# Optimization experiments

Hardware: AMD Instinct MI355X
Metric: run time of the kernel (lower is better)

## Reference

```python
import jax, jax.numpy as jnp
import numpy as np

EPS_LN = 1e-5
EPS_BN = 1e-5
NUM_HEADS = 8


def _gelu(x):
    return jax.nn.gelu(x, approximate=False)


def _ln(x, w, b):
    # LayerNorm over last (channel) dim, eps=1e-5 (torch default)
    mu = jnp.mean(x, axis=-1, keepdims=True)
    var = jnp.mean((x - mu) ** 2, axis=-1, keepdims=True)
    return (x - mu) / jnp.sqrt(var + EPS_LN) * w + b


def _bn(x, g, b):
    # eval-mode BatchNorm2d on NCHW with running_mean=0, running_var=1
    scale = g * (1.0 + EPS_BN) ** -0.5
    return x * scale[None, :, None, None] + b[None, :, None, None]


def _conv1x1(x, w):
    # x: [B,C,H,W], w: [O,C]
    return jnp.einsum('bchw,oc->bohw', x, w)


def _unfold3(x, r):
    # nn.Unfold(kernel=3, dilation=r, padding=r): gather 3x3 dilated neighborhoods
    B, C, H, W = x.shape
    xp = jnp.pad(x, ((0, 0), (0, 0), (r, r), (r, r)))
    pats = [xp[:, :, i * r:i * r + H, j * r:j * r + W] for i in range(3) for j in range(3)]
    return jnp.stack(pats, axis=2)  # [B,C,9,H,W]


def _atrous_attn(q, k, v, num_heads, r):
    # per-pixel local attention: q [B,C,H,W] attends to 9 dilated neighbors of k/v
    B, C, H, W = q.shape
    hd = C // num_heads
    scale = hd ** -0.5
    qh = q.reshape(B, num_heads, hd, H, W)
    kp = _unfold3(k, r).reshape(B, num_heads, hd, 9, H, W)
    attn = jax.nn.softmax(jnp.einsum('bnchw,bnckhw->bnkhw', qh, kp) * scale, axis=2)
    vp = _unfold3(v, r).reshape(B, num_heads, hd, 9, H, W)
    out = jnp.einsum('bnkhw,bnckhw->bnchw', attn, vp)
    return out.reshape(B, C, H, W).transpose(0, 2, 3, 1)  # [B,H,W,C]


def _window_attn(x_bhwc, qkv_w, proj_w, proj_b, num_heads, r):
    xc = x_bhwc.transpose(0, 3, 1, 2)
    C = xc.shape[1]
    qkv = _conv1x1(xc, qkv_w)  # [B,3C,H,W], order q|k|v
    out = _atrous_attn(qkv[:, :C], qkv[:, C:2 * C], qkv[:, 2 * C:], num_heads, r)
    return jnp.einsum('bhwc,oc->bhwo', out, proj_w) + proj_b


def _mlp(x_bhwc, c1_w, c1_b, bn1_g, bn1_b, dw_w, dw_b, bn2_g, bn2_b, c2_w, c2_b, bn3_g, bn3_b):
    xc = x_bhwc.transpose(0, 3, 1, 2)
    h = _bn(_gelu(_conv1x1(xc, c1_w) + c1_b[None, :, None, None]), bn1_g, bn1_b)
    dw = jax.lax.conv_general_dilated(h, dw_w, (1, 1), 'SAME',
                                      feature_group_count=h.shape[1],
                                      dimension_numbers=('NCHW', 'OIHW', 'NCHW'))
    dw = dw + dw_b[None, :, None, None]
    h = _bn(_gelu(dw + h), bn2_g, bn2_b)
    out = _bn(_conv1x1(h, c2_w) + c2_b[None, :, None, None], bn3_g, bn3_b)
    return out.transpose(0, 2, 3, 1)


def reference(x, ln1_w, ln1_b, ln2_w, ln2_b,
              qkv1_w, proj1_w, proj1_b, qkv2_w, proj2_w, proj2_b, qkv3_w, proj3_w, proj3_b,
              tc_conv_w, tc_conv_b, tc_bn1_g, tc_bn1_b, tc_pool_w, tc_bn2_g, tc_bn2_b,
              tc_trans_w, tc_trans_b, tc_bn3_g, tc_bn3_b,
              mlp_c1_w, mlp_c1_b, mlp_bn1_g, mlp_bn1_b, mlp_dw_w, mlp_dw_b,
              mlp_bn2_g, mlp_bn2_b, mlp_c2_w, mlp_c2_b, mlp_bn3_g, mlp_bn3_b):
    tx = x.transpose(0, 2, 3, 1)  # [B,H,W,C]
    n1 = _ln(tx, ln1_w, ln1_b)
    t1 = tx + _window_attn(n1, qkv1_w, proj1_w, proj1_b, NUM_HEADS, 1)
    t2 = tx + _window_attn(n1, qkv2_w, proj2_w, proj2_b, NUM_HEADS, 2)
    t3 = tx + _window_attn(n1, qkv3_w, proj3_w, proj3_b, NUM_HEADS, 3)
    # Trans_conv: ASPP-style fusion
    xc1 = jax.nn.relu(_bn(_conv1x1(x, tc_conv_w) + tc_conv_b[None, :, None, None], tc_bn1_g, tc_bn1_b))
    pool = jnp.mean(x, axis=(2, 3), keepdims=True)
    pool = jax.nn.relu(_bn(_conv1x1(pool, tc_pool_w), tc_bn2_g, tc_bn2_b))
    pool = jnp.broadcast_to(pool, x.shape)  # bilinear upsample of a 1x1 map == broadcast
    cat = jnp.concatenate([xc1, t1.transpose(0, 3, 1, 2), t2.transpose(0, 3, 1, 2),
                           t3.transpose(0, 3, 1, 2), pool], axis=1)  # [B,5C,H,W]
    tr = jax.nn.relu(_bn(_conv1x1(cat, tc_trans_w) + tc_trans_b[None, :, None, None],
                         tc_bn3_g, tc_bn3_b)).transpose(0, 2, 3, 1)  # [B,H,W,C]
    tr = tr + _mlp(_ln(tr, ln2_w, ln2_b), mlp_c1_w, mlp_c1_b, mlp_bn1_g, mlp_bn1_b,
                   mlp_dw_w, mlp_dw_b, mlp_bn2_g, mlp_bn2_b, mlp_c2_w, mlp_c2_b,
                   mlp_bn3_g, mlp_bn3_b)
    return tr.transpose(0, 3, 1, 2)  # [B,C,H,W]


def setup_inputs():
    key = jax.random.key(0)
    B, C, H, W = 4, 256, 64, 64
    HID = 4 * C
    ks = iter(jax.random.split(key, 64))

    def nrm(shape, scale=0.02):
        return jax.random.normal(next(ks), shape, dtype=jnp.float32) * scale

    inp = {
        'x': jax.random.normal(next(ks), (B, C, H, W), dtype=jnp.float32),
        'ln1_w': jnp.ones((C,), jnp.float32), 'ln1_b': jnp.zeros((C,), jnp.float32),
        'ln2_w': jnp.ones((C,), jnp.float32), 'ln2_b': jnp.zeros((C,), jnp.float32),
    }
    for i in (1, 2, 3):
        inp[f'qkv{i}_w'] = nrm((3 * C, C))
        inp[f'proj{i}_w'] = nrm((C, C))
        inp[f'proj{i}_b'] = jnp.zeros((C,), jnp.float32)
    inp.update(
        tc_conv_w=nrm((C, C)), tc_conv_b=jnp.zeros((C,), jnp.float32),
        tc_bn1_g=jnp.ones((C,), jnp.float32), tc_bn1_b=jnp.zeros((C,), jnp.float32),
        tc_pool_w=nrm((C, C)),
        tc_bn2_g=jnp.ones((C,), jnp.float32), tc_bn2_b=jnp.zeros((C,), jnp.float32),
        tc_trans_w=nrm((C, 5 * C)), tc_trans_b=jnp.zeros((C,), jnp.float32),
        tc_bn3_g=jnp.ones((C,), jnp.float32), tc_bn3_b=jnp.zeros((C,), jnp.float32),
        mlp_c1_w=nrm((HID, C)), mlp_c1_b=jnp.zeros((HID,), jnp.float32),
        mlp_bn1_g=jnp.ones((HID,), jnp.float32), mlp_bn1_b=jnp.zeros((HID,), jnp.float32),
        mlp_dw_w=nrm((HID, 1, 3, 3), 0.1), mlp_dw_b=jnp.zeros((HID,), jnp.float32),
        mlp_bn2_g=jnp.ones((HID,), jnp.float32), mlp_bn2_b=jnp.zeros((HID,), jnp.float32),
        mlp_c2_w=nrm((C, HID)), mlp_c2_b=jnp.zeros((C,), jnp.float32),
        mlp_bn3_g=jnp.ones((C,), jnp.float32), mlp_bn3_b=jnp.zeros((C,), jnp.float32),
    )
    return inp
```

## Files before the change

### kernel.cpp

```cpp
#include <hip/hip_runtime.h>

#define N_PIX 16384
#define CDIM  256
#define HIDD  1024
#define BNS   0.9999950000374997f

typedef __attribute__((ext_vector_type(8))) short  short8;
typedef __attribute__((ext_vector_type(4))) float  f32x4;
typedef __attribute__((ext_vector_type(4))) int    int4v;
typedef __attribute__((ext_vector_type(2))) int    int2v;

__device__ __forceinline__ float b2f(unsigned short u){
  unsigned int x = ((unsigned int)u) << 16; float f;
  __builtin_memcpy(&f, &x, 4); return f;
}
__device__ __forceinline__ unsigned short f2b(float f){
  unsigned int x; __builtin_memcpy(&x, &f, 4);
  unsigned int r = (x + 0x7fffu + ((x >> 16) & 1u)) >> 16;
  return (unsigned short)r;
}
__device__ __forceinline__ float geluf(float x){
  return 0.5f * x * (1.0f + erff(x * 0.70710678118654752f));
}

typedef const __attribute__((address_space(1))) unsigned int* gas_t;
typedef __attribute__((address_space(3))) unsigned int*       las_t;
__device__ __forceinline__ void gload16(const void* g, void* l){
  __builtin_amdgcn_global_load_lds((gas_t)g, (las_t)l, 16, 0, 0);
}

__global__ __launch_bounds__(256) void k_cvt_all(
    const float* __restrict__ s0, const float* __restrict__ s1, const float* __restrict__ s2,
    const float* __restrict__ s3, const float* __restrict__ s4, const float* __restrict__ s5,
    const float* __restrict__ s6, const float* __restrict__ s7, const float* __restrict__ s8,
    const float* __restrict__ s9, unsigned short* __restrict__ wb){
  const float* srcs[10] = {s0,s1,s2,s3,s4,s5,s6,s7,s8,s9};
  const int n[10]   = {196608,196608,196608,65536,65536,65536,65536,327680,262144,262144};
  const int off[10] = {0,196608,393216,589824,655360,720896,786432,851968,1179648,1441792};
  int seg = blockIdx.y;
  int i = (blockIdx.x * 256 + threadIdx.x) * 8;
  if (i >= n[seg]) return;
  const float* src = srcs[seg];
  unsigned short* dst = wb + off[seg];
  f32x4 a = *(const f32x4*)(src + i);
  f32x4 b = *(const f32x4*)(src + i + 4);
  unsigned short o[8];
  #pragma unroll
  for (int j = 0; j < 4; ++j){ o[j] = f2b(a[j]); o[4 + j] = f2b(b[j]); }
  *(int4v*)(dst + i) = *(int4v*)o;
}

__global__ __launch_bounds__(256) void k_dwwT(const float* __restrict__ dww,
                                              unsigned short* __restrict__ dwwT){
  int i = blockIdx.x * 256 + threadIdx.x;
  if (i >= 9216) return;
  int kk = i >> 10, c = i & 1023;
  dwwT[i] = f2b(dww[c * 9 + kk]);
}

__global__ __launch_bounds__(256) void k_transpose(const float* __restrict__ x,
                                                   unsigned short* __restrict__ xpm,
                                                   float* __restrict__ xpm32){
  __shared__ __align__(16) float tile[64][65];
  int b = blockIdx.z, c0 = blockIdx.y * 64, p0 = blockIdx.x * 64;
  int t = threadIdx.x;
  int r = t >> 3, k = t & 7;
  for (int s = 0; s < 2; ++s){
    int rr = r + s * 32;
    const float* src = x + (((size_t)(b * CDIM + c0 + rr)) << 12) + p0 + k * 8;
    f32x4 a = *(const f32x4*)src;
    f32x4 c = *(const f32x4*)(src + 4);
    #pragma unroll
    for (int j = 0; j < 4; ++j){ tile[rr][k * 8 + j] = a[j]; tile[rr][k * 8 + 4 + j] = c[j]; }
  }
  __syncthreads();
  for (int s = 0; s < 2; ++s){
    int pr = r + s * 32;
    float tf[8];
    unsigned short tb[8];
    #pragma unroll
    for (int j = 0; j < 8; ++j){ tf[j] = tile[k * 8 + j][pr]; tb[j] = f2b(tf[j]); }
    size_t rowoff = ((size_t)(b * 4096 + p0 + pr)) << 8;
    *(int4v*)(xpm + rowoff + c0 + k * 8) = *(int4v*)tb;
    *(f32x4*)(xpm32 + rowoff + c0 + k * 8)     = *(f32x4*)&tf[0];
    *(f32x4*)(xpm32 + rowoff + c0 + k * 8 + 4) = *(f32x4*)&tf[4];
  }
}

template<typename IT>
__global__ __launch_bounds__(256) void k_ln(const IT* __restrict__ in,
    const float* __restrict__ w, const float* __restrict__ bia,
    unsigned short* __restrict__ out){
  int row  = blockIdx.x * 4 + (threadIdx.x >> 6);
  int lane = threadIdx.x & 63;
  float v[4];
  const IT* p = in + (size_t)row * CDIM + lane * 4;
  if constexpr (sizeof(IT) == 2){
    int2v d = *(const int2v*)p;
    unsigned short tmp[4]; __builtin_memcpy(tmp, &d, 8);
    #pragma unroll
    for (int j = 0; j < 4; ++j) v[j] = b2f(tmp[j]);
  } else {
    f32x4 d = *(const f32x4*)p;
    #pragma unroll
    for (int j = 0; j < 4; ++j) v[j] = d[j];
  }
  float s  = v[0] + v[1] + v[2] + v[3];
  float s2 = v[0]*v[0] + v[1]*v[1] + v[2]*v[2] + v[3]*v[3];
  #pragma unroll
  for (int m = 1; m < 64; m <<= 1){
    s  += __shfl_xor(s,  m);
    s2 += __shfl_xor(s2, m);
  }
  float mu   = s * (1.0f / 256.0f);
  float var  = s2 * (1.0f / 256.0f) - mu * mu;
  float rstd = rsqrtf(var + 1e-5f);
  unsigned short o[4];
  #pragma unroll
  for (int j = 0; j < 4; ++j){
    int c = lane * 4 + j;
    o[j] = f2b((v[j] - mu) * rstd * w[c] + bia[c]);
  }
  *(int2v*)(out + (size_t)row * CDIM + lane * 4) = *(int2v*)o;
}

template<int MODE>
__global__ __launch_bounds__(256) void k_gemm(
    const unsigned short* __restrict__ A, const unsigned short* __restrict__ Bw,
    int K, int Nout, int ldb, void* __restrict__ outp,
    const float* __restrict__ bias,
    const float* __restrict__ bng,
    const float* __restrict__ bnb,
    const float* __restrict__ auxf,
    int catoff)
{
  __shared__ __align__(16) unsigned short As[2][64 * 32];
  __shared__ __align__(16) unsigned short Bs[2][128 * 32];
  int t = threadIdx.x;
  int m0 = blockIdx.y * 64, n0 = blockIdx.x * 128;
  int lane = t & 63;
  int w  = __builtin_amdgcn_readfirstlane(t >> 6);
  int wm = w >> 1, wn = w & 1;
  int lr = lane & 15, kb = lane >> 4;

  f32x4 acc[2][4];
  f32x4 z = {0.f, 0.f, 0.f, 0.f};
  #pragma unroll
  for (int i = 0; i < 2; ++i)
    #pragma unroll
    for (int j = 0; j < 4; ++j) acc[i][j] = z;

  int srow = lane >> 2, schunk = (lane & 3) * 8;
  const unsigned short* gA  = A  + (size_t)(m0 + w * 16 + srow) * K   + schunk;
  const unsigned short* gB0 = Bw + (size_t)(n0 + w * 16 + srow) * ldb + schunk;
  const unsigned short* gB1 = Bw + (size_t)(n0 + 64 + w * 16 + srow) * ldb + schunk;

  const int nt = K >> 5;
  gload16(gA,  As[0] + w * 512);
  gload16(gB0, Bs[0] + w * 512);
  gload16(gB1, Bs[0] + 2048 + w * 512);
  __syncthreads();

  for (int tt = 0; tt < nt; ++tt){
    int cur = tt & 1;
    if (tt + 1 < nt){
      int k1 = (tt + 1) << 5;
      gload16(gA  + k1, As[cur ^ 1] + w * 512);
      gload16(gB0 + k1, Bs[cur ^ 1] + w * 512);
      gload16(gB1 + k1, Bs[cur ^ 1] + 2048 + w * 512);
    }
    short8 af[2], bf_[4];
    #pragma unroll
    for (int i = 0; i < 2; ++i)
      af [i] = *(const short8*)&As[cur][(wm * 32 + i * 16 + lr) * 32 + kb * 8];
    #pragma unroll
    for (int j = 0; j < 4; ++j)
      bf_[j] = *(const short8*)&Bs[cur][(wn * 64 + j * 16 + lr) * 32 + kb * 8];
    #pragma unroll
    for (int i = 0; i < 2; ++i)
      #pragma unroll
      for (int j = 0; j < 4; ++j)
        acc[i][j] = __builtin_amdgcn_mfma_f32_16x16x32_bf16(af[i], bf_[j], acc[i][j], 0, 0, 0);
    __syncthreads();
  }

  #pragma unroll
  for (int i = 0; i < 2; ++i){
    int rowb = m0 + wm * 32 + i * 16 + kb * 4;
    #pragma unroll
    for (int j = 0; j < 4; ++j){
      int col = n0 + wn * 64 + j * 16 + lr;
      #pragma unroll
      for (int rr = 0; rr < 4; ++rr){
        int row = rowb + rr;
        float v = acc[i][j][rr];
        if constexpr (MODE == 0){
          ((unsigned short*)outp)[(size_t)row * Nout + col] = f2b(v);
        } else if constexpr (MODE == 1){
          v += bias[col] + auxf[(size_t)row * CDIM + col];
          ((unsigned short*)outp)[(size_t)row * HIDD + catoff + col] = f2b(v);
        } else if constexpr (MODE == 2){
          v = (v + bias[col]) * (bng[col] * BNS) + bnb[col];
          v = fmaxf(v, 0.0f);
          ((unsigned short*)outp)[(size_t)row * HIDD + col] = f2b(v);
        } else if constexpr (MODE == 3){
          v += bias[col] + auxf[((row >> 12) << 8) + col];
          v = v * (bng[col] * BNS) + bnb[col];
          v = fmaxf(v, 0.0f);
          ((float*)outp)[(size_t)row * CDIM + col] = v;
        } else if constexpr (MODE == 4){
          v = geluf(v + bias[col]);
          v = v * (bng[col] * BNS) + bnb[col];
          ((unsigned short*)outp)[(size_t)row * HIDD + col] = f2b(v);
        } else {
          v = (v + bias[col]) * (bng[col] * BNS) + bnb[col];
          v += auxf[(size_t)row * CDIM + col];
          int b = row >> 12, hw = row & 4095;
          ((float*)outp)[(((size_t)(b * CDIM + col)) << 12) + hw] = v;
        }
      }
    }
  }
}

__global__ __launch_bounds__(256) void k_attn(const unsigned short* __restrict__ QKV,
                                              unsigned short* __restrict__ ATT, int r){
  int t = blockIdx.x * 256 + threadIdx.x;
  int head = t & 7, pix = t >> 3;
  int hw = pix & 4095, h = hw >> 6, w = hw & 63;
  const unsigned short* base = QKV + (size_t)pix * 768 + head * 32;

  float q[32];
  #pragma unroll
  for (int c8 = 0; c8 < 4; ++c8){
    int4v d = *(const int4v*)(base + c8 * 8);
    unsigned short tmp[8]; __builtin_memcpy(tmp, &d, 16);
    #pragma unroll
    for (int j = 0; j < 8; ++j) q[c8 * 8 + j] = b2f(tmp[j]);
  }
  float logit[9];
  #pragma unroll
  for (int jj = 0; jj < 9; ++jj){
    int dh = (jj / 3 - 1) * r, dw = (jj % 3 - 1) * r;
    int hh = h + dh, ww = w + dw;
    float d = 0.0f;
    if (hh >= 0 && hh < 64 && ww >= 0 && ww < 64){
      const unsigned short* kr = base + (dh * 64 + dw) * 768 + 256;
      #pragma unroll
      for (int c8 = 0; c8 < 4; ++c8){
        int4v dd = *(const int4v*)(kr + c8 * 8);
        unsigned short tmp[8]; __builtin_memcpy(tmp, &dd, 16);
        #pragma unroll
        for (int j = 0; j < 8; ++j) d += q[c8 * 8 + j] * b2f(tmp[j]);
      }
    }
    logit[jj] = d * 0.17677669529663687f;
  }
  float m = logit[0];
  #pragma unroll
  for (int jj = 1; jj < 9; ++jj) m = fmaxf(m, logit[jj]);
  float p[9], s = 0.0f;
  #pragma unroll
  for (int jj = 0; jj < 9; ++jj){ p[jj] = __expf(logit[jj] - m); s += p[jj]; }
  float inv = 1.0f / s;
  float o[32];
  #pragma unroll
  for (int j = 0; j < 32; ++j) o[j] = 0.0f;
  #pragma unroll
  for (int jj = 0; jj < 9; ++jj){
    int dh = (jj / 3 - 1) * r, dw = (jj % 3 - 1) * r;
    int hh = h + dh, ww = w + dw;
    if (hh >= 0 && hh < 64 && ww >= 0 && ww < 64){
      float pj = p[jj] * inv;
      const unsigned short* vr = base + (dh * 64 + dw) * 768 + 512;
      #pragma unroll
      for (int c8 = 0; c8 < 4; ++c8){
        int4v dd = *(const int4v*)(vr + c8 * 8);
        unsigned short tmp[8]; __builtin_memcpy(tmp, &dd, 16);
        #pragma unroll
        for (int j = 0; j < 8; ++j) o[c8 * 8 + j] += pj * b2f(tmp[j]);
      }
    }
  }
  unsigned short ob[32];
  #pragma unroll
  for (int j = 0; j < 32; ++j) ob[j] = f2b(o[j]);
  unsigned short* op = ATT + (size_t)pix * CDIM + head * 32;
  #pragma unroll
  for (int c8 = 0; c8 < 4; ++c8) *(int4v*)(op + c8 * 8) = *(int4v*)&ob[c8 * 8];
}

__global__ __launch_bounds__(256) void k_dwconv(const unsigned short* __restrict__ H,
    const unsigned short* __restrict__ dwwT, const float* __restrict__ dwb,
    const float* __restrict__ g, const float* __restrict__ bb,
    unsigned short* __restrict__ H2){
  int t = blockIdx.x * 256 + threadIdx.x;
  int chunk = t & 127, pix = t >> 7;
  int hw = pix & 4095, h = hw >> 6, w = hw & 63;
  int c0 = chunk * 8;
  float acc[8], hc[8];
  {
    int4v dd = *(const int4v*)(H + (size_t)pix * HIDD + c0);
    unsigned short tmp[8]; __builtin_memcpy(tmp, &dd, 16);
    #pragma unroll
    for (int j = 0; j < 8; ++j){ hc[j] = b2f(tmp[j]); acc[j] = 0.0f; }
  }
  #pragma unroll
  for (int di = -1; di <= 1; ++di)
    #pragma unroll
    for (int dj = -1; dj <= 1; ++dj){
      int hh = h + di, ww = w + dj;
      if (hh < 0 || hh >= 64 || ww < 0 || ww >= 64) continue;
      int kk = (di + 1) * 3 + (dj + 1);
      int4v dd = *(const int4v*)(H + ((size_t)(pix + di * 64 + dj)) * HIDD + c0);
      int4v wv = *(const int4v*)(dwwT + kk * 1024 + c0);
      unsigned short tmp[8], wt[8];
      __builtin_memcpy(tmp, &dd, 16);
      __builtin_memcpy(wt,  &wv, 16);
      #pragma unroll
      for (int j = 0; j < 8; ++j) acc[j] += b2f(wt[j]) * b2f(tmp[j]);
    }
  f32x4 bv0 = *(const f32x4*)(dwb + c0), bv1 = *(const f32x4*)(dwb + c0 + 4);
  f32x4 gv0 = *(const f32x4*)(g   + c0), gv1 = *(const f32x4*)(g   + c0 + 4);
  f32x4 cv0 = *(const f32x4*)(bb  + c0), cv1 = *(const f32x4*)(bb  + c0 + 4);
  float bvv[8], gvv[8], cvv[8];
  #pragma unroll
  for (int j = 0; j < 4; ++j){
    bvv[j] = bv0[j]; bvv[4 + j] = bv1[j];
    gvv[j] = gv0[j]; gvv[4 + j] = gv1[j];
    cvv[j] = cv0[j]; cvv[4 + j] = cv1[j];
  }
  unsigned short ob[8];
  #pragma unroll
  for (int j = 0; j < 8; ++j){
    float v = acc[j] + bvv[j] + hc[j];
    v = geluf(v);
    v = v * (gvv[j] * BNS) + cvv[j];
    ob[j] = f2b(v);
  }
  *(int4v*)(H2 + (size_t)pix * HIDD + c0) = *(int4v*)ob;
}

__global__ __launch_bounds__(256) void k_pool_mean(const float* __restrict__ x,
                                                   float* __restrict__ pm){
  int bc = blockIdx.x;
  const float* p = x + ((size_t)bc << 12);
  int t = threadIdx.x;
  float s = 0.0f;
  for (int i = t * 4; i < 4096; i += 1024){
    f32x4 dd = *(const f32x4*)(p + i);
    s += dd[0] + dd[1] + dd[2] + dd[3];
  }
  #pragma unroll
  for (int m = 1; m < 64; m <<= 1) s += __shfl_xor(s, m);
  __shared__ float red[4];
  if ((t & 63) == 0) red[t >> 6] = s;
  __syncthreads();
  if (t == 0) pm[bc] = (red[0] + red[1] + red[2] + red[3]) * (1.0f / 4096.0f);
}

__global__ __launch_bounds__(256) void k_poolfb(const float* __restrict__ pm,
    const float* __restrict__ pw, const float* __restrict__ g,
    const float* __restrict__ bb, const float* __restrict__ tw,
    float* __restrict__ pb){
  int b = blockIdx.x, o = threadIdx.x;
  __shared__ float v[256];
  __shared__ float pfs[256];
  v[o] = pm[b * 256 + o];
  __syncthreads();
  float acc = 0.0f;
  const float* wr = pw + (size_t)o * 256;
  for (int c = 0; c < 256; ++c) acc += v[c] * wr[c];
  float val = acc * (g[o] * BNS) + bb[o];
  pfs[o] = fmaxf(val, 0.0f);
  __syncthreads();
  float acc2 = 0.0f;
  const float* tr = tw + (size_t)o * 1280 + 1024;
  for (int c = 0; c < 256; ++c) acc2 += pfs[c] * tr[c];
  pb[b * 256 + o] = acc2;
}

extern "C" void kernel_launch(void* const* d_in, const int* in_sizes, int n_in,
                              void* d_out, int out_size, void* d_ws, size_t ws_size,
                              hipStream_t stream){
  const float* x     = (const float*)d_in[0];
  const float* ln1w  = (const float*)d_in[1];
  const float* ln1b  = (const float*)d_in[2];
  const float* ln2w  = (const float*)d_in[3];
  const float* ln2b  = (const float*)d_in[4];
  const float* qkvw[3]  = {(const float*)d_in[5], (const float*)d_in[8],  (const float*)d_in[11]};
  const float* projw[3] = {(const float*)d_in[6], (const float*)d_in[9],  (const float*)d_in[12]};
  const float* projb[3] = {(const float*)d_in[7], (const float*)d_in[10], (const float*)d_in[13]};
  const float* tcw   = (const float*)d_in[14];
  const float* tcb   = (const float*)d_in[15];
  const float* bn1g  = (const float*)d_in[16];
  const float* bn1b  = (const float*)d_in[17];
  const float* poolw = (const float*)d_in[18];
  const float* bn2g  = (const float*)d_in[19];
  const float* bn2b  = (const float*)d_in[20];
  const float* trw   = (const float*)d_in[21];
  const float* trb   = (const float*)d_in[22];
  const float* bn3g  = (const float*)d_in[23];
  const float* bn3b  = (const float*)d_in[24];
  const float* c1w   = (const float*)d_in[25];
  const float* c1b   = (const float*)d_in[26];
  const float* mbn1g = (const float*)d_in[27];
  const float* mbn1b = (const float*)d_in[28];
  const float* dww   = (const float*)d_in[29];
  const float* dwb   = (const float*)d_in[30];
  const float* mbn2g = (const float*)d_in[31];
  const float* mbn2b = (const float*)d_in[32];
  const float* c2w   = (const float*)d_in[33];
  const float* c2b   = (const float*)d_in[34];
  const float* mbn3g = (const float*)d_in[35];
  const float* mbn3b = (const float*)d_in[36];

  char* ws = (char*)d_ws;
  unsigned short* Xpm = (unsigned short*)(ws);
  unsigned short* N1  = (unsigned short*)(ws + 8388608);
  unsigned short* CAT = (unsigned short*)(ws + 16777216);
  float*          TR  = (float*)        (ws + 50331648);
  float*          Xpm32 = TR;
  unsigned short* E   = (unsigned short*)(ws + 67108864);
  unsigned short* F   = (unsigned short*)(ws + 100663296);
  unsigned short* Wb    = (unsigned short*)(ws + 134217728);
  unsigned short* qkvb[3]  = {Wb, Wb + 196608, Wb + 393216};
  unsigned short* projbw[3] = {Wb + 589824, Wb + 655360, Wb + 720896};
  unsigned short* tcwb  = Wb + 786432;
  unsigned short* trwb  = Wb + 851968;
  unsigned short* c1wb  = Wb + 1179648;
  unsigned short* c2wb  = Wb + 1441792;
  unsigned short* dwwT  = Wb + 1703936;
  float*          pm  = (float*)(ws + 134217728 + 3428352);
  float*          pb  = pm + 1024;

  k_cvt_all<<<dim3(160, 10), 256, 0, stream>>>(qkvw[0], qkvw[1], qkvw[2],
                                               projw[0], projw[1], projw[2],
                                               tcw, trw, c1w, c2w, Wb);
  k_dwwT<<<36, 256, 0, stream>>>(dww, dwwT);

  k_transpose<<<dim3(64, 4, 4), 256, 0, stream>>>(x, Xpm, Xpm32);
  k_pool_mean<<<1024, 256, 0, stream>>>(x, pm);
  k_ln<unsigned short><<<4096, 256, 0, stream>>>(Xpm, ln1w, ln1b, N1);
  k_poolfb<<<4, 256, 0, stream>>>(pm, poolw, bn2g, bn2b, trw, pb);

  for (int i = 0; i < 3; ++i){
    k_gemm<0><<<dim3(6, 256), 256, 0, stream>>>(N1, qkvb[i], 256, 768, 256, E,
                                                nullptr, nullptr, nullptr, nullptr, 0);
    k_attn<<<512, 256, 0, stream>>>(E, F, i + 1);
    k_gemm<1><<<dim3(2, 256), 256, 0, stream>>>(F, projbw[i], 256, 256, 256, CAT,
                                                projb[i], nullptr, nullptr, Xpm32,
                                                (i + 1) * 256);
  }
  k_gemm<2><<<dim3(2, 256), 256, 0, stream>>>(Xpm, tcwb, 256, 256, 256, CAT,
                                              tcb, bn1g, bn1b, nullptr, 0);
  k_gemm<3><<<dim3(2, 256), 256, 0, stream>>>(CAT, trwb, 1024, 256, 1280, TR,
                                              trb, bn3g, bn3b, pb, 0);
  k_ln<float><<<4096, 256, 0, stream>>>(TR, ln2w, ln2b, N1);
  k_gemm<4><<<dim3(8, 256), 256, 0, stream>>>(N1, c1wb, 256, 1024, 256, E,
                                              c1b, mbn1g, mbn1b, nullptr, 0);
  k_dwconv<<<8192, 256, 0, stream>>>(E, dwwT, dwb, mbn2g, mbn2b, F);
  k_gemm<5><<<dim3(2, 256), 256, 0, stream>>>(F, c2wb, 1024, 256, 1024, d_out,
                                              c2b, mbn3g, mbn3b, TR, 0);
}
```

Baseline: 428.8 us.

## Batch three attention branches into single QKV GEMM, attention and grouped projection launches

Replaces the per-branch loop of QKV GEMM, attention and projection GEMM with one wide QKV GEMM producing all three branches, one attention launch covering all dilations, and one grouped GEMM that also covers the tc_conv branch. It also folds the channel-mean pooling into the transpose kernel with atomics, zeroing the accumulator inside the dwwT kernel. The aim is fewer launches and larger grids that fill the GPU better, at the cost of larger intermediate buffers and atomic reductions.

```diff
diff --git a/kernel.cpp b/kernel.cpp
--- a/kernel.cpp
+++ b/kernel.cpp
@@ -51,8 +51,10 @@
 }
 
 __global__ __launch_bounds__(256) void k_dwwT(const float* __restrict__ dww,
-                                              unsigned short* __restrict__ dwwT){
+                                              unsigned short* __restrict__ dwwT,
+                                              float* __restrict__ pm){
   int i = blockIdx.x * 256 + threadIdx.x;
+  if (i < 1024) pm[i] = 0.0f;
   if (i >= 9216) return;
   int kk = i >> 10, c = i & 1023;
   dwwT[i] = f2b(dww[c * 9 + kk]);
@@ -60,18 +62,27 @@
 
 __global__ __launch_bounds__(256) void k_transpose(const float* __restrict__ x,
                                                    unsigned short* __restrict__ xpm,
-                                                   float* __restrict__ xpm32){
+                                                   float* __restrict__ xpm32,
+                                                   float* __restrict__ pm){
   __shared__ __align__(16) float tile[64][65];
   int b = blockIdx.z, c0 = blockIdx.y * 64, p0 = blockIdx.x * 64;
   int t = threadIdx.x;
   int r = t >> 3, k = t & 7;
+  float psum[2];
   for (int s = 0; s < 2; ++s){
     int rr = r + s * 32;
     const float* src = x + (((size_t)(b * CDIM + c0 + rr)) << 12) + p0 + k * 8;
     f32x4 a = *(const f32x4*)src;
     f32x4 c = *(const f32x4*)(src + 4);
+    psum[s] = a[0] + a[1] + a[2] + a[3] + c[0] + c[1] + c[2] + c[3];
     #pragma unroll
     for (int j = 0; j < 4; ++j){ tile[rr][k * 8 + j] = a[j]; tile[rr][k * 8 + 4 + j] = c[j]; }
+  }
+  #pragma unroll
+  for (int s = 0; s < 2; ++s){
+    float v = psum[s];
+    v += __shfl_xor(v, 1); v += __shfl_xor(v, 2); v += __shfl_xor(v, 4);
+    if ((t & 7) == 0) atomicAdd(&pm[b * 256 + c0 + r + s * 32], v);
   }
   __syncthreads();
   for (int s = 0; s < 2; ++s){
@@ -196,13 +207,6 @@
         float v = acc[i][j][rr];
         if constexpr (MODE == 0){
           ((unsigned short*)outp)[(size_t)row * Nout + col] = f2b(v);
-        } else if constexpr (MODE == 1){
-          v += bias[col] + auxf[(size_t)row * CDIM + col];
-          ((unsigned short*)outp)[(size_t)row * HIDD + catoff + col] = f2b(v);
-        } else if constexpr (MODE == 2){
-          v = (v + bias[col]) * (bng[col] * BNS) + bnb[col];
-          v = fmaxf(v, 0.0f);
-          ((unsigned short*)outp)[(size_t)row * HIDD + col] = f2b(v);
         } else if constexpr (MODE == 3){
           v += bias[col] + auxf[((row >> 12) << 8) + col];
           v = v * (bng[col] * BNS) + bnb[col];
@@ -223,12 +227,105 @@
   }
 }
 
-__global__ __launch_bounds__(256) void k_attn(const unsigned short* __restrict__ QKV,
-                                              unsigned short* __restrict__ ATT, int r){
-  int t = blockIdx.x * 256 + threadIdx.x;
+struct GrpArgs {
+  const unsigned short* A[4];
+  const unsigned short* B[4];
+  const float* bias[4];
+  int lda[4];
+  int catoff[4];
+};
+
+__global__ __launch_bounds__(256) void k_gemm_grp(GrpArgs ga,
+    const float* __restrict__ xpm32, const float* __restrict__ bng,
+    const float* __restrict__ bnb, unsigned short* __restrict__ CAT)
+{
+  __shared__ __align__(16) unsigned short As[2][64 * 32];
+  __shared__ __align__(16) unsigned short Bs[2][128 * 32];
+  int t = threadIdx.x;
+  int g  = blockIdx.x >> 1;
+  int n0 = (blockIdx.x & 1) * 128;
+  int m0 = blockIdx.y * 64;
+  const unsigned short* A  = ga.A[g];
+  const unsigned short* Bw = ga.B[g];
+  const float* bias = ga.bias[g];
+  int lda = ga.lda[g];
+  int catoff = ga.catoff[g];
+
+  int lane = t & 63;
+  int w  = __builtin_amdgcn_readfirstlane(t >> 6);
+  int wm = w >> 1, wn = w & 1;
+  int lr = lane & 15, kb = lane >> 4;
+
+  f32x4 acc[2][4];
+  f32x4 z = {0.f, 0.f, 0.f, 0.f};
+  #pragma unroll
+  for (int i = 0; i < 2; ++i)
+    #pragma unroll
+    for (int j = 0; j < 4; ++j) acc[i][j] = z;
+
+  int srow = lane >> 2, schunk = (lane & 3) * 8;
+  const unsigned short* gA  = A  + (size_t)(m0 + w * 16 + srow) * lda + schunk;
+  const unsigned short* gB0 = Bw + (size_t)(n0 + w * 16 + srow) * 256 + schunk;
+  const unsigned short* gB1 = Bw + (size_t)(n0 + 64 + w * 16 + srow) * 256 + schunk;
+
+  gload16(gA,  As[0] + w * 512);
+  gload16(gB0, Bs[0] + w * 512);
+  gload16(gB1, Bs[0] + 2048 + w * 512);
+  __syncthreads();
+
+  for (int tt = 0; tt < 8; ++tt){
+    int cur = tt & 1;
+    if (tt + 1 < 8){
+      int k1 = (tt + 1) << 5;
+      gload16(gA  + k1, As[cur ^ 1] + w * 512);
+      gload16(gB0 + k1, Bs[cur ^ 1] + w * 512);
+      gload16(gB1 + k1, Bs[cur ^ 1] + 2048 + w * 512);
+    }
+    short8 af[2], bf_[4];
+    #pragma unroll
+    for (int i = 0; i < 2; ++i)
+      af [i] = *(const short8*)&As[cur][(wm * 32 + i * 16 + lr) * 32 + kb * 8];
+    #pragma unroll
+    for (int j = 0; j < 4; ++j)
+      bf_[j] = *(const short8*)&Bs[cur][(wn * 64 + j * 16 + lr) * 32 + kb * 8];
+    #pragma unroll
+    for (int i = 0; i < 2; ++i)
+      #pragma unroll
+      for (int j = 0; j < 4; ++j)
+        acc[i][j] = __builtin_amdgcn_mfma_f32_16x16x32_bf16(af[i], bf_[j], acc[i][j], 0, 0, 0);
+    __syncthreads();
+  }
+
+  #pragma unroll
+  for (int i = 0; i < 2; ++i){
+    int rowb = m0 + wm * 32 + i * 16 + kb * 4;
+    #pragma unroll
+    for (int j = 0; j < 4; ++j){
+      int col = n0 + wn * 64 + j * 16 + lr;
+      #pragma unroll
+      for (int rr = 0; rr < 4; ++rr){
+        int row = rowb + rr;
+        float v = acc[i][j][rr];
+        if (g == 3){
+          v = (v + bias[col]) * (bng[col] * BNS) + bnb[col];
+          v = fmaxf(v, 0.0f);
+        } else {
+          v += bias[col] + xpm32[(size_t)row * CDIM + col];
+        }
+        CAT[(size_t)row * HIDD + catoff + col] = f2b(v);
+      }
+    }
+  }
+}
+
+__global__ __launch_bounds__(256) void k_attn3(const unsigned short* __restrict__ QKV3,
+                                               unsigned short* __restrict__ F3){
+  int grp = blockIdx.x >> 9;
+  int r = grp + 1;
+  int t = (blockIdx.x & 511) * 256 + threadIdx.x;
   int head = t & 7, pix = t >> 3;
   int hw = pix & 4095, h = hw >> 6, w = hw & 63;
-  const unsigned short* base = QKV + (size_t)pix * 768 + head * 32;
+  const unsigned short* base = QKV3 + (size_t)pix * 2304 + grp * 768 + head * 32;
 
   float q[32];
   #pragma unroll
@@ -245,7 +342,7 @@
     int hh = h + dh, ww = w + dw;
     float d = 0.0f;
     if (hh >= 0 && hh < 64 && ww >= 0 && ww < 64){
-      const unsigned short* kr = base + (dh * 64 + dw) * 768 + 256;
+      const unsigned short* kr = base + (dh * 64 + dw) * 2304 + 256;
       #pragma unroll
       for (int c8 = 0; c8 < 4; ++c8){
         int4v dd = *(const int4v*)(kr + c8 * 8);
@@ -272,7 +369,7 @@
     int hh = h + dh, ww = w + dw;
     if (hh >= 0 && hh < 64 && ww >= 0 && ww < 64){
       float pj = p[jj] * inv;
-      const unsigned short* vr = base + (dh * 64 + dw) * 768 + 512;
+      const unsigned short* vr = base + (dh * 64 + dw) * 2304 + 512;
       #pragma unroll
       for (int c8 = 0; c8 < 4; ++c8){
         int4v dd = *(const int4v*)(vr + c8 * 8);
@@ -285,7 +382,7 @@
   unsigned short ob[32];
   #pragma unroll
   for (int j = 0; j < 32; ++j) ob[j] = f2b(o[j]);
-  unsigned short* op = ATT + (size_t)pix * CDIM + head * 32;
+  unsigned short* op = F3 + (size_t)pix * 768 + grp * 256 + head * 32;
   #pragma unroll
   for (int c8 = 0; c8 < 4; ++c8) *(int4v*)(op + c8 * 8) = *(int4v*)&ob[c8 * 8];
 }
@@ -341,24 +438,6 @@
   *(int4v*)(H2 + (size_t)pix * HIDD + c0) = *(int4v*)ob;
 }
 
-__global__ __launch_bounds__(256) void k_pool_mean(const float* __restrict__ x,
-                                                   float* __restrict__ pm){
-  int bc = blockIdx.x;
-  const float* p = x + ((size_t)bc << 12);
-  int t = threadIdx.x;
-  float s = 0.0f;
-  for (int i = t * 4; i < 4096; i += 1024){
-    f32x4 dd = *(const f32x4*)(p + i);
-    s += dd[0] + dd[1] + dd[2] + dd[3];
-  }
-  #pragma unroll
-  for (int m = 1; m < 64; m <<= 1) s += __shfl_xor(s, m);
-  __shared__ float red[4];
-  if ((t & 63) == 0) red[t >> 6] = s;
-  __syncthreads();
-  if (t == 0) pm[bc] = (red[0] + red[1] + red[2] + red[3]) * (1.0f / 4096.0f);
-}
-
 __global__ __launch_bounds__(256) void k_poolfb(const float* __restrict__ pm,
     const float* __restrict__ pw, const float* __restrict__ g,
     const float* __restrict__ bb, const float* __restrict__ tw,
@@ -366,7 +445,7 @@
   int b = blockIdx.x, o = threadIdx.x;
   __shared__ float v[256];
   __shared__ float pfs[256];
-  v[o] = pm[b * 256 + o];
+  v[o] = pm[b * 256 + o] * (1.0f / 4096.0f);
   __syncthreads();
   float acc = 0.0f;
   const float* wr = pw + (size_t)o * 256;
@@ -421,10 +500,9 @@
   unsigned short* CAT = (unsigned short*)(ws + 16777216);
   float*          TR  = (float*)        (ws + 50331648);
   float*          Xpm32 = TR;
-  unsigned short* E   = (unsigned short*)(ws + 67108864);
-  unsigned short* F   = (unsigned short*)(ws + 100663296);
-  unsigned short* Wb    = (unsigned short*)(ws + 134217728);
-  unsigned short* qkvb[3]  = {Wb, Wb + 196608, Wb + 393216};
+  unsigned short* H   = (unsigned short*)(ws + 67108864);
+  unsigned short* H2  = (unsigned short*)(ws + 100663296);
+  unsigned short* Wb  = (unsigned short*)(ws + 134217728);
   unsigned short* projbw[3] = {Wb + 589824, Wb + 655360, Wb + 720896};
   unsigned short* tcwb  = Wb + 786432;
   unsigned short* trwb  = Wb + 851968;
@@ -433,33 +511,35 @@
   unsigned short* dwwT  = Wb + 1703936;
   float*          pm  = (float*)(ws + 134217728 + 3428352);
   float*          pb  = pm + 1024;
+  unsigned short* E3  = (unsigned short*)(ws + 140509184);
+  unsigned short* F3  = (unsigned short*)(ws + 216006656);
 
   k_cvt_all<<<dim3(160, 10), 256, 0, stream>>>(qkvw[0], qkvw[1], qkvw[2],
                                                projw[0], projw[1], projw[2],
                                                tcw, trw, c1w, c2w, Wb);
-  k_dwwT<<<36, 256, 0, stream>>>(dww, dwwT);
-
-  k_transpose<<<dim3(64, 4, 4), 256, 0, stream>>>(x, Xpm, Xpm32);
-  k_pool_mean<<<1024, 256, 0, stream>>>(x, pm);
+  k_dwwT<<<36, 256, 0, stream>>>(dww, dwwT, pm);
+  k_transpose<<<dim3(64, 4, 4), 256, 0, stream>>>(x, Xpm, Xpm32, pm);
   k_ln<unsigned short><<<4096, 256, 0, stream>>>(Xpm, ln1w, ln1b, N1);
   k_poolfb<<<4, 256, 0, stream>>>(pm, poolw, bn2g, bn2b, trw, pb);
 
-  for (int i = 0; i < 3; ++i){
-    k_gemm<0><<<dim3(6, 256), 256, 0, stream>>>(N1, qkvb[i], 256, 768, 256, E,
-                                                nullptr, nullptr, nullptr, nullptr, 0);
-    k_attn<<<512, 256, 0, stream>>>(E, F, i + 1);
-    k_gemm<1><<<dim3(2, 256), 256, 0, stream>>>(F, projbw[i], 256, 256, 256, CAT,
-                                                projb[i], nullptr, nullptr, Xpm32,
-                                                (i + 1) * 256);
-  }
-  k_gemm<2><<<dim3(2, 256), 256, 0, stream>>>(Xpm, tcwb, 256, 256, 256, CAT,
-                                              tcb, bn1g, bn1b, nullptr, 0);
+  k_gemm<0><<<dim3(18, 256), 256, 0, stream>>>(N1, Wb, 256, 2304, 256, E3,
+                                               nullptr, nullptr, nullptr, nullptr, 0);
+  k_attn3<<<1536, 256, 0, stream>>>(E3, F3);
+  {
+    GrpArgs ga;
+    ga.A[0] = F3;       ga.A[1] = F3 + 256; ga.A[2] = F3 + 512; ga.A[3] = Xpm;
+    ga.B[0] = projbw[0]; ga.B[1] = projbw[1]; ga.B[2] = projbw[2]; ga.B[3] = tcwb;
+    ga.bias[0] = projb[0]; ga.bias[1] = projb[1]; ga.bias[2] = projb[2]; ga.bias[3] = tcb;
+    ga.lda[0] = 768; ga.lda[1] = 768; ga.lda[2] = 768; ga.lda[3] = 256;
+    ga.catoff[0] = 256; ga.catoff[1] = 512; ga.catoff[2] = 768; ga.catoff[3] = 0;
+    k_gemm_grp<<<dim3(8, 256), 256, 0, stream>>>(ga, Xpm32, bn1g, bn1b, CAT);
+  }
   k_gemm<3><<<dim3(2, 256), 256, 0, stream>>>(CAT, trwb, 1024, 256, 1280, TR,
                                               trb, bn3g, bn3b, pb, 0);
   k_ln<float><<<4096, 256, 0, stream>>>(TR, ln2w, ln2b, N1);
-  k_gemm<4><<<dim3(8, 256), 256, 0, stream>>>(N1, c1wb, 256, 1024, 256, E,
+  k_gemm<4><<<dim3(8, 256), 256, 0, stream>>>(N1, c1wb, 256, 1024, 256, H,
                                               c1b, mbn1g, mbn1b, nullptr, 0);
-  k_dwconv<<<8192, 256, 0, stream>>>(E, dwwT, dwb, mbn2g, mbn2b, F);
-  k_gemm<5><<<dim3(2, 256), 256, 0, stream>>>(F, c2wb, 1024, 256, 1024, d_out,
+  k_dwconv<<<8192, 256, 0, stream>>>(H, dwwT, dwb, mbn2g, mbn2b, H2);
+  k_gemm<5><<<dim3(2, 256), 256, 0, stream>>>(H2, c2wb, 1024, 256, 1024, d_out,
                                               c2b, mbn3g, mbn3b, TR, 0);
 }
```

After: 425.3 us. Within noise of the previous version (-0.8%).
